# Kernel optimization log

Measured on AMD Instinct MI355X. Metric: run time of the kernel, lower is better.

## Reference

```python
import jax, jax.numpy as jnp
import numpy as np

VOCAB = 50257   # N_max = len(word_to_idx)
IN_DIM = 256
HID = 13        # forced: out Linear in_features = 2*hidden_dim must equal dec output 2*13
L = 2048


def _lstm_dir(seq, Wih, Whh, b, reverse):
    """Single-direction LSTM over seq [T, F] with zero init. b = b_ih + b_hh.
    Torch gate order: i, f, g, o."""
    H = Whh.shape[1]

    def step(carry, x_t):
        h, c = carry
        z = Wih @ x_t + Whh @ h + b                  # (4H,)
        i, f, g, o = jnp.split(z, 4)
        c2 = jax.nn.sigmoid(f) * c + jax.nn.sigmoid(i) * jnp.tanh(g)
        h2 = jax.nn.sigmoid(o) * jnp.tanh(c2)
        return (h2, c2), h2

    init = (jnp.zeros((H,), seq.dtype), jnp.zeros((H,), seq.dtype))
    (hn, cn), hs = jax.lax.scan(step, init, seq, reverse=reverse)
    return hs, hn, cn


def _dec_cell(x_scalar, h, c, Wih, Whh, b):
    """One LSTM cell step with scalar input (input_size=1). Returns new h."""
    z = Wih[:, 0] * x_scalar + Whh @ h + b
    i, f, g, o = jnp.split(z, 4)
    c2 = jax.nn.sigmoid(f) * c + jax.nn.sigmoid(i) * jnp.tanh(g)
    return jax.nn.sigmoid(o) * jnp.tanh(c2)


def setup_inputs() -> dict:
    key = jax.random.key(0)
    ks = jax.random.split(key, 16)
    s = 0.05
    G = 4 * HID  # 52; also num_layers*2*HID = 52 (proj in_features)
    return {
        "x": jax.random.randint(ks[0], (L,), 0, VOCAB),
        "emb_W": jax.random.normal(ks[1], (VOCAB + 1, IN_DIM)) * s,
        "enc_Wih0": jax.random.normal(ks[2], (2, G, IN_DIM)) * s,   # [dir, 4H, in]
        "enc_Whh0": jax.random.normal(ks[3], (2, G, HID)) * s,
        "enc_b0": jax.random.normal(ks[4], (2, G)) * s,
        "enc_Wih1": jax.random.normal(ks[5], (2, G, 2 * HID)) * s,  # layer1 input = 2*HID
        "enc_Whh1": jax.random.normal(ks[6], (2, G, HID)) * s,
        "enc_b1": jax.random.normal(ks[7], (2, G)) * s,
        "proj1_W": jax.random.normal(ks[8], (2 * HID, 2 * 2 * HID)) * s,
        "proj1_b": jax.random.normal(ks[9], (2 * HID,)) * s,
        "proj2_W": jax.random.normal(ks[10], (2 * HID, 2 * 2 * HID)) * s,
        "proj2_b": jax.random.normal(ks[11], (2 * HID,)) * s,
        "dec_Wih": jax.random.normal(ks[12], (2, G, 1)) * s,
        "dec_Whh": jax.random.normal(ks[13], (2, G, HID)) * s,
        "dec_b": jax.random.normal(ks[14], (2, G)) * s,
        "out_W": jax.random.normal(ks[15], (VOCAB, 2 * HID)) * s,
        "out_b": jnp.zeros((VOCAB,), jnp.float32),
    }


def reference(x, emb_W, enc_Wih0, enc_Whh0, enc_b0, enc_Wih1, enc_Whh1, enc_b1,
              proj1_W, proj1_b, proj2_W, proj2_b, dec_Wih, dec_Whh, dec_b,
              out_W, out_b):
    embs = emb_W[x]                                            # (L, IN_DIM)

    # Encoder: 2-layer bidirectional LSTM, batch=1 (vectors).
    hs_f0, hnf0, cnf0 = _lstm_dir(embs, enc_Wih0[0], enc_Whh0[0], enc_b0[0], False)
    hs_b0, hnb0, cnb0 = _lstm_dir(embs, enc_Wih0[1], enc_Whh0[1], enc_b0[1], True)
    out0 = jnp.concatenate([hs_f0, hs_b0], axis=-1)            # (L, 2*HID)
    _, hnf1, cnf1 = _lstm_dir(out0, enc_Wih1[0], enc_Whh1[0], enc_b1[0], False)
    _, hnb1, cnb1 = _lstm_dir(out0, enc_Wih1[1], enc_Whh1[1], enc_b1[1], True)

    # torch h_n layout: [l0_fwd, l0_bwd, l1_fwd, l1_bwd]
    h_flat = jnp.concatenate([hnf0, hnb0, hnf1, hnb1])         # (52,)
    c_flat = jnp.concatenate([cnf0, cnb0, cnf1, cnb1])
    state_h = (proj1_W @ h_flat + proj1_b).reshape(2, HID)     # dec (dir, HID) init
    state_c = (proj2_W @ c_flat + proj2_b).reshape(2, HID)

    # Decoder step 0: input -1.0 with projected initial state.
    start = jnp.float32(-1.0)
    step0 = jnp.concatenate([
        _dec_cell(start, state_h[0], state_c[0], dec_Wih[0], dec_Whh[0], dec_b[0]),
        _dec_cell(start, state_h[1], state_c[1], dec_Wih[1], dec_Whh[1], dec_b[1]),
    ])                                                          # (26,)

    # Steps i>0: original code calls self.dec(input) with NO hidden state, so each
    # step uses zero initial state and depends only on x[i-1] -> fully parallel.
    xs = x[:-1].astype(jnp.float32)                             # (L-1,)
    z0 = jnp.zeros((HID,), jnp.float32)
    rest = jax.vmap(lambda v: jnp.concatenate([
        _dec_cell(v, z0, z0, dec_Wih[0], dec_Whh[0], dec_b[0]),
        _dec_cell(v, z0, z0, dec_Wih[1], dec_Whh[1], dec_b[1]),
    ]))(xs)                                                     # (L-1, 26)

    dec_out = jnp.concatenate([step0[None, :], rest], axis=0)   # (L, 26)
    preds = dec_out @ out_W.T + out_b                           # (L, VOCAB)
    return preds, embs
```

## Files before the change

### kernel.cpp

```cpp
#include <hip/hip_runtime.h>
#include <hip/hip_bf16.h>
#include <cstdint>
#include <cstddef>

#define L      2048
#define IN_DIM 256
#define HID    13
#define G      52
#define VOCAB  50257
#define PRED_N ((size_t)L * VOCAB)
#define L2E    1.4426950408889634f
#define INV2L2E 0.34657359027997264f
#define NTX    50
#define NTILE  (NTX * 16)
#define GB     254

static __device__ __forceinline__ float fexp2(float x) { return __builtin_amdgcn_exp2f(x); }
static __device__ __forceinline__ float frcp(float x) { return __builtin_amdgcn_rcpf(x); }
static __device__ __forceinline__ float sigm(float z) { return 1.f - frcp(fexp2(z * L2E) + 1.f); }
static __device__ __forceinline__ float tanh_(float z) { return 1.f - 2.f * frcp(fexp2(z * (2.f * L2E)) + 1.f); }
static __device__ __forceinline__ float bcast(float v, int l) {
    return __int_as_float(__builtin_amdgcn_readlane(__float_as_int(v), l));
}

__global__ void __launch_bounds__(64) k_probe_dep(float* __restrict__ o)
{
    float a = 1.0f + threadIdx.x * 1e-6f;
    #pragma unroll 16
    for (int i = 0; i < 4096; ++i) a = fmaf(a, 1.0000001f, 1e-9f);
    o[threadIdx.x] = a;
}
__global__ void __launch_bounds__(64) k_probe_ilp(float* __restrict__ o)
{
    float a0 = 1.f, a1 = 1.1f, a2 = 1.2f, a3 = 1.3f, a4 = 1.4f, a5 = 1.5f, a6 = 1.6f, a7 = 1.7f;
    #pragma unroll 8
    for (int i = 0; i < 512; ++i) {
        a0 = fmaf(a0, 1.0000001f, 1e-9f); a1 = fmaf(a1, 1.0000001f, 1e-9f);
        a2 = fmaf(a2, 1.0000001f, 1e-9f); a3 = fmaf(a3, 1.0000001f, 1e-9f);
        a4 = fmaf(a4, 1.0000001f, 1e-9f); a5 = fmaf(a5, 1.0000001f, 1e-9f);
        a6 = fmaf(a6, 1.0000001f, 1e-9f); a7 = fmaf(a7, 1.0000001f, 1e-9f);
    }
    o[64 + threadIdx.x] = ((a0 + a1) + (a2 + a3)) + ((a4 + a5) + (a6 + a7));
}

__global__ void __launch_bounds__(160) k_emb_u0(
    const int* __restrict__ x, const float* __restrict__ embW,
    const float* __restrict__ Wih0, const float* __restrict__ b0,
    const float* __restrict__ dWih, const float* __restrict__ db,
    float* __restrict__ out_embs, float* __restrict__ u0, float* __restrict__ dec)
{
    __shared__ float se[IN_DIM];
    int t = blockIdx.x;
    int tid = threadIdx.x;
    if (tid < 128) {
        int rowx = x[t];
        float2 e = ((const float2*)(embW + (size_t)rowx * IN_DIM))[tid];
        se[2 * tid]     = e.x;
        se[2 * tid + 1] = e.y;
        ((float2*)(out_embs + (size_t)t * IN_DIM))[tid] = e;
    }
    __syncthreads();
    if (tid < 2 * G) {
        int dirg = tid / G, g = tid % G;
        int gate = g / HID, row = g % HID;
        float msc = (gate == 2) ? 2.f * L2E : L2E;
        float acc = b0[dirg * G + g];
        const float* w = Wih0 + (size_t)(dirg * G + g) * IN_DIM;
        #pragma unroll 8
        for (int k = 0; k < IN_DIM; ++k)
            acc = fmaf(w[k], se[k], acc);
        u0[((size_t)dirg * L + t) * 64 + gate * 16 + row] = msc * acc;
    } else if (tid < 128) {
        int p = tid - 2 * G;
        int dirp = p / 12, pp = p % 12;
        int gate = pp / 3, row = HID + pp % 3;
        u0[((size_t)dirp * L + t) * 64 + gate * 16 + row] = 0.f;
    } else if (tid < 128 + 2 * HID && t >= 1) {
        int j = tid - 128;
        int dir = j / HID, jj = j % HID;
        float v = (float)x[t - 1];
        int base = dir * G;
        float zi = fmaf(dWih[base + jj],           v, db[base + jj]);
        float zg = fmaf(dWih[base + 2 * HID + jj], v, db[base + 2 * HID + jj]);
        float zo = fmaf(dWih[base + 3 * HID + jj], v, db[base + 3 * HID + jj]);
        float c2 = sigm(zi) * tanh_(zg);
        dec[(size_t)t * (2 * HID) + j] = sigm(zo) * tanh_(c2);
    }
}

static __device__ __forceinline__ void compute8(
    const float* buf, const float* whh, float kcv, float onev,
    bool m16, bool m32, float& h, float& c, float* h8)
{
    #pragma unroll
    for (int k = 0; k < 8; ++k) {
        float h0 = bcast(h, 0), h1 = bcast(h, 1), h2 = bcast(h, 2), h3 = bcast(h, 3);
        float h4 = bcast(h, 4), h5 = bcast(h, 5), h6 = bcast(h, 6), h7 = bcast(h, 7);
        float h8_ = bcast(h, 8), h9 = bcast(h, 9), h10 = bcast(h, 10), h11 = bcast(h, 11);
        float h12 = bcast(h, 12);
        float A = fmaf(whh[0], h0, buf[k]);
        float B = whh[1] * h1;
        A = fmaf(whh[2],  h2,  A);  B = fmaf(whh[3],  h3,  B);
        A = fmaf(whh[4],  h4,  A);  B = fmaf(whh[5],  h5,  B);
        A = fmaf(whh[6],  h6,  A);  B = fmaf(whh[7],  h7,  B);
        A = fmaf(whh[8],  h8_, A);  B = fmaf(whh[9],  h9,  B);
        A = fmaf(whh[10], h10, A);  B = fmaf(whh[11], h11, B);
        A = fmaf(whh[12], h12, A);
        float z = A + B;
        float act = fmaf(-kcv, frcp(fexp2(z) + 1.f), onev);
        float pa = act, pb = act;
        asm("s_nop 1\n\tv_permlane16_swap_b32 %0, %1" : "+v"(pa), "+v"(pb));
        float sf = m16 ? pa : pb;
        float qa = act, qb = act;
        asm("s_nop 1\n\tv_permlane32_swap_b32 %0, %1" : "+v"(qa), "+v"(qb));
        float tg = m32 ? qa : qb;
        float ra = tg, rb = tg;
        asm("s_nop 1\n\tv_permlane16_swap_b32 %0, %1" : "+v"(ra), "+v"(rb));
        float so = m16 ? ra : rb;
        float c2 = fmaf(sf, c, act * tg);
        float th = fmaf(-2.f, frcp(fexp2(c2) + 1.f), 1.f);
        h = so * th;
        c = c2;
        h8[k] = h;
    }
}

template<bool DOUT>
static __device__ __forceinline__ void chain_core(
    const float* ub, int pstep, const float* whh, float kcv, float onev,
    bool m16, bool m32, float* outp, float& hout, float& cout)
{
    float bufA[8], bufB[8], h8[8];
    float h = 0.f, c = 0.f;
    #pragma unroll
    for (int k = 0; k < 8; ++k) bufA[k] = ub[k * pstep];
    #pragma unroll
    for (int k = 0; k < 8; ++k) bufB[k] = ub[(8 + k) * pstep];

    for (int tcb = 0; tcb < L; tcb += 16) {
        compute8(bufA, whh, kcv, onev, m16, m32, h, c, h8);
        if (DOUT) {
            #pragma unroll
            for (int k = 0; k < 8; ++k) outp[k * pstep] = h8[k];
            outp += 8 * pstep;
        }
        if (tcb + 16 < L) {
            #pragma unroll
            for (int k = 0; k < 8; ++k) bufA[k] = ub[(tcb + 16 + k) * pstep];
        }
        compute8(bufB, whh, kcv, onev, m16, m32, h, c, h8);
        if (DOUT) {
            #pragma unroll
            for (int k = 0; k < 8; ++k) outp[k * pstep] = h8[k];
            outp += 8 * pstep;
        }
        if (tcb + 24 < L) {
            #pragma unroll
            for (int k = 0; k < 8; ++k) bufB[k] = ub[(tcb + 24 + k) * pstep];
        }
    }
    hout = h; cout = c;
}

template<bool DOUT>
static __device__ __forceinline__ void run_chain(
    const float* u, const float* Whh, float* out0p,
    float* finh, float* finc, int chain_base, int dir, int lane)
{
    int lg16 = lane & 15, gate = lane >> 4;
    int rsrc = gate * HID + (lg16 < HID ? lg16 : HID - 1);
    float kcv, onev;
    if (gate == 2)      { kcv = 2.f;        onev = 1.f; }
    else if (gate == 0) { kcv = 2.f * L2E;  onev = 2.f * L2E; }
    else                { kcv = 1.f;        onev = 1.f; }
    float msc = (gate == 2) ? 2.f * L2E : L2E;
    float whh[HID];
    #pragma unroll
    for (int k = 0; k < HID; ++k) whh[k] = msc * Whh[(dir * G + rsrc) * HID + k];

    int ia = lane, ib = lane;
    asm("s_nop 1\n\tv_permlane16_swap_b32 %0, %1" : "+v"(ia), "+v"(ib));
    bool m16 = (ia == (lane ^ 16));
    int ja = lane, jb = lane;
    asm("s_nop 1\n\tv_permlane32_swap_b32 %0, %1" : "+v"(ja), "+v"(jb));
    bool m32 = (ja == (lane ^ 32));

    const float* ub = u + (size_t)dir * L * 64 + (dir ? (size_t)(L - 1) * 64 : 0) + lane;
    int pstep = dir ? -64 : 64;
    float* outp = out0p ? out0p + ((size_t)dir * L + (dir ? L - 1 : 0)) * 64 + lane : (float*)nullptr;

    float h, c;
    chain_core<DOUT>(ub, pstep, whh, kcv, onev, m16, m32, outp, h, c);

    if (lane < HID) {
        finh[(chain_base + dir) * HID + lane] = h;
        finc[(chain_base + dir) * HID + lane] = c * INV2L2E;
    }
}

__global__ void __launch_bounds__(512) k_phase0(
    const float* __restrict__ u, const float* __restrict__ Whh,
    float* __restrict__ out0p, float* __restrict__ finh, float* __restrict__ finc,
    const float* __restrict__ dec, const float* __restrict__ outW,
    const float* __restrict__ outb, float* __restrict__ preds)
{
    __shared__ float sd[128][28];
    int bid = blockIdx.x;
    int tid = threadIdx.x;
    if (bid < 2) {
        if (tid >= 64) return;
        __builtin_amdgcn_s_setprio(3);
        run_chain<true>(u, Whh, out0p, finh, finc, 0, bid, tid);
        return;
    }
    __builtin_amdgcn_s_setprio(0);
    int b = bid - 2;
    const int q = NTILE / GB, r = NTILE % GB;
    int start = b * q + (b < r ? b : r);
    int cnt   = q + (b < r ? 1 : 0);
    for (int tt = 0; tt < cnt; ++tt) {
        int tile = start + tt;
        int ix = tile % NTX, iy = tile / NTX;
        int nbase = ix * 1024, i0 = iy * 128;
        __syncthreads();
        for (int li = tid; li < 128 * 26; li += 512) {
            int rr = li / 26, cc = li % 26;
            sd[rr][cc] = dec[(size_t)(i0 + rr) * 26 + cc];
        }
        __syncthreads();
        int n0 = nbase + tid, n1 = nbase + 512 + tid;
        bool a0 = n0 < VOCAB, a1 = n1 < VOCAB;
        float w0[26], w1[26], b0v = 0.f, b1v = 0.f;
        #pragma unroll
        for (int k = 0; k < 26; ++k) { w0[k] = 0.f; w1[k] = 0.f; }
        if (a0) { const float* w = outW + (size_t)n0 * 26;
            #pragma unroll
            for (int k = 0; k < 26; ++k) w0[k] = w[k];
            b0v = outb[n0]; }
        if (a1) { const float* w = outW + (size_t)n1 * 26;
            #pragma unroll
            for (int k = 0; k < 26; ++k) w1[k] = w[k];
            b1v = outb[n1]; }
        for (int i = 0; i < 128; ++i) {
            int grow = i0 + i;
            float acc0 = b0v, acc1 = b1v;
            const float* dr = sd[i];
            #pragma unroll
            for (int k = 0; k < 26; ++k) {
                float d = dr[k];
                acc0 = fmaf(d, w0[k], acc0);
                acc1 = fmaf(d, w1[k], acc1);
            }
            if (grow != 0) {
                size_t rb = (size_t)grow * VOCAB;
                if (a0) preds[rb + n0] = acc0;
                if (a1) preds[rb + n1] = acc1;
            }
        }
    }
}

__global__ void k_u1(const float* __restrict__ out0p, const float* __restrict__ Wih1,
                     const float* __restrict__ b1, float* __restrict__ u1)
{
    int idx = blockIdx.x * blockDim.x + threadIdx.x;
    if (idx >= L * 2 * 64) return;
    int t    = idx >> 7;
    int remv = idx & 127;
    int d1   = remv >> 6;
    int lane = remv & 63;
    int gate = lane >> 4, row = lane & 15;
    size_t oidx = ((size_t)d1 * L + t) * 64 + lane;
    if (row >= HID) { u1[oidx] = 0.f; return; }
    int g = gate * HID + row;
    float msc = (gate == 2) ? 2.f * L2E : L2E;
    float acc = b1[d1 * G + g];
    const float* w = Wih1 + (size_t)(d1 * G + g) * (2 * HID);
    const float* o0 = out0p + (size_t)t * 64;
    const float* o1 = out0p + ((size_t)L + t) * 64;
    #pragma unroll
    for (int k = 0; k < HID; ++k)
        acc = fmaf(w[k], o0[k], acc);
    #pragma unroll
    for (int k = 0; k < HID; ++k)
        acc = fmaf(w[HID + k], o1[k], acc);
    u1[oidx] = msc * acc;
}

__global__ void __launch_bounds__(64) k_phase1(
    const float* __restrict__ u, const float* __restrict__ Whh,
    float* __restrict__ finh, float* __restrict__ finc)
{
    run_chain<false>(u, Whh, (float*)nullptr, finh, finc, 2, blockIdx.x, threadIdx.x);
}

__global__ void __launch_bounds__(64) k_final(const float* __restrict__ fin_h, const float* __restrict__ fin_c,
                                              const float* __restrict__ p1W, const float* __restrict__ p1b,
                                              const float* __restrict__ p2W, const float* __restrict__ p2b,
                                              const float* __restrict__ dWih, const float* __restrict__ dWhh,
                                              const float* __restrict__ db, float* __restrict__ dec)
{
    __shared__ float sh[2 * HID], sc[2 * HID], sz[G];
    int tid = threadIdx.x;
    if (tid < 4 * HID) {
        int r = tid < 2 * HID ? tid : tid - 2 * HID;
        const float* W   = tid < 2 * HID ? p1W : p2W;
        const float* src = tid < 2 * HID ? fin_h : fin_c;
        float acc = tid < 2 * HID ? p1b[r] : p2b[r];
        for (int k = 0; k < 4 * HID; ++k) acc = fmaf(W[r * 4 * HID + k], src[k], acc);
        if (tid < 2 * HID) sh[r] = acc; else sc[r] = acc;
    }
    __syncthreads();
    for (int dir = 0; dir < 2; ++dir) {
        if (tid < G) {
            float acc = db[dir * G + tid] - dWih[dir * G + tid];
            for (int k = 0; k < HID; ++k)
                acc = fmaf(dWhh[(dir * G + tid) * HID + k], sh[dir * HID + k], acc);
            sz[tid] = acc;
        }
        __syncthreads();
        if (tid < HID) {
            float si = sigm(sz[tid]);
            float sf = sigm(sz[HID + tid]);
            float tg = tanh_(sz[2 * HID + tid]);
            float so = sigm(sz[3 * HID + tid]);
            float c2 = fmaf(sf, sc[dir * HID + tid], si * tg);
            dec[dir * HID + tid] = so * tanh_(c2);
        }
        __syncthreads();
    }
}

__global__ void k_row0(const float* __restrict__ dec, const float* __restrict__ outW,
                       const float* __restrict__ outb, float* __restrict__ preds)
{
    int n = blockIdx.x * blockDim.x + threadIdx.x;
    if (n >= VOCAB) return;
    float acc = outb[n];
    const float* w = outW + (size_t)n * 26;
    #pragma unroll
    for (int k = 0; k < 26; ++k) acc = fmaf(w[k], dec[k], acc);
    preds[n] = acc;
}

extern "C" void kernel_launch(void* const* d_in, const int* in_sizes, int n_in,
                              void* d_out, int out_size, void* d_ws, size_t ws_size,
                              hipStream_t stream)
{
    (void)in_sizes; (void)n_in; (void)out_size; (void)ws_size;

    const int*   x     = (const int*)d_in[0];
    const float* embW  = (const float*)d_in[1];
    const float* eWih0 = (const float*)d_in[2];
    const float* eWhh0 = (const float*)d_in[3];
    const float* eb0   = (const float*)d_in[4];
    const float* eWih1 = (const float*)d_in[5];
    const float* eWhh1 = (const float*)d_in[6];
    const float* eb1   = (const float*)d_in[7];
    const float* p1W   = (const float*)d_in[8];
    const float* p1b   = (const float*)d_in[9];
    const float* p2W   = (const float*)d_in[10];
    const float* p2b   = (const float*)d_in[11];
    const float* dWih  = (const float*)d_in[12];
    const float* dWhh  = (const float*)d_in[13];
    const float* db    = (const float*)d_in[14];
    const float* outW  = (const float*)d_in[15];
    const float* outb  = (const float*)d_in[16];

    float* ws    = (float*)d_ws;
    float* u0    = ws;
    float* u1    = u0 + 2 * L * 64;
    float* out0p = u1 + 2 * L * 64;
    float* dec   = out0p + 2 * L * 64;
    float* fin_h = dec + L * 2 * HID;
    float* fin_c = fin_h + 64;
    float* probe = fin_c + 64;

    float* preds    = (float*)d_out;
    float* out_embs = preds + PRED_N;

    hipLaunchKernelGGL(k_probe_dep, dim3(1), dim3(64), 0, stream, probe);
    hipLaunchKernelGGL(k_probe_ilp, dim3(1), dim3(64), 0, stream, probe);

    hipLaunchKernelGGL(k_emb_u0, dim3(L), dim3(160), 0, stream,
                       x, embW, eWih0, eb0, dWih, db, out_embs, u0, dec);

    hipLaunchKernelGGL(k_phase0, dim3(2 + GB), dim3(512), 0, stream,
                       u0, eWhh0, out0p, fin_h, fin_c,
                       dec, outW, outb, preds);

    hipLaunchKernelGGL(k_u1, dim3((L * 2 * 64 + 255) / 256), dim3(256), 0, stream,
                       out0p, eWih1, eb1, u1);

    hipLaunchKernelGGL(k_phase1, dim3(2), dim3(64), 0, stream,
                       u1, eWhh1, fin_h, fin_c);

    hipLaunchKernelGGL(k_final, dim3(1), dim3(64), 0, stream,
                       fin_h, fin_c, p1W, p1b, p2W, p2b, dWih, dWhh, db, dec);

    hipLaunchKernelGGL(k_row0, dim3((VOCAB + 255) / 256), dim3(256), 0, stream,
                       dec, outW, outb, preds);
}
```

Measured before the change: 617.2 us.

## Remove probe kernels, widen phase0 blocks, split recurrence FMA chain

```diff
diff --git a/kernel.cpp b/kernel.cpp
--- a/kernel.cpp
+++ b/kernel.cpp
@@ -11,9 +11,10 @@
 #define PRED_N ((size_t)L * VOCAB)
 #define L2E    1.4426950408889634f
 #define INV2L2E 0.34657359027997264f
-#define NTX    50
+#define NTX    25
 #define NTILE  (NTX * 16)
 #define GB     254
+#define DYNLDS 49152
 
 static __device__ __forceinline__ float fexp2(float x) { return __builtin_amdgcn_exp2f(x); }
 static __device__ __forceinline__ float frcp(float x) { return __builtin_amdgcn_rcpf(x); }
@@ -21,26 +22,6 @@
 static __device__ __forceinline__ float tanh_(float z) { return 1.f - 2.f * frcp(fexp2(z * (2.f * L2E)) + 1.f); }
 static __device__ __forceinline__ float bcast(float v, int l) {
     return __int_as_float(__builtin_amdgcn_readlane(__float_as_int(v), l));
-}
-
-__global__ void __launch_bounds__(64) k_probe_dep(float* __restrict__ o)
-{
-    float a = 1.0f + threadIdx.x * 1e-6f;
-    #pragma unroll 16
-    for (int i = 0; i < 4096; ++i) a = fmaf(a, 1.0000001f, 1e-9f);
-    o[threadIdx.x] = a;
-}
-__global__ void __launch_bounds__(64) k_probe_ilp(float* __restrict__ o)
-{
-    float a0 = 1.f, a1 = 1.1f, a2 = 1.2f, a3 = 1.3f, a4 = 1.4f, a5 = 1.5f, a6 = 1.6f, a7 = 1.7f;
-    #pragma unroll 8
-    for (int i = 0; i < 512; ++i) {
-        a0 = fmaf(a0, 1.0000001f, 1e-9f); a1 = fmaf(a1, 1.0000001f, 1e-9f);
-        a2 = fmaf(a2, 1.0000001f, 1e-9f); a3 = fmaf(a3, 1.0000001f, 1e-9f);
-        a4 = fmaf(a4, 1.0000001f, 1e-9f); a5 = fmaf(a5, 1.0000001f, 1e-9f);
-        a6 = fmaf(a6, 1.0000001f, 1e-9f); a7 = fmaf(a7, 1.0000001f, 1e-9f);
-    }
-    o[64 + threadIdx.x] = ((a0 + a1) + (a2 + a3)) + ((a4 + a5) + (a6 + a7));
 }
 
 __global__ void __launch_bounds__(160) k_emb_u0(
@@ -88,9 +69,10 @@
     }
 }
 
+template<bool DOUT>
 static __device__ __forceinline__ void compute8(
     const float* buf, const float* whh, float kcv, float onev,
-    bool m16, bool m32, float& h, float& c, float* h8)
+    bool m16, bool m32, float& h, float& c, float* outp, int pstep)
 {
     #pragma unroll
     for (int k = 0; k < 8; ++k) {
@@ -100,13 +82,14 @@
         float h12 = bcast(h, 12);
         float A = fmaf(whh[0], h0, buf[k]);
         float B = whh[1] * h1;
-        A = fmaf(whh[2],  h2,  A);  B = fmaf(whh[3],  h3,  B);
-        A = fmaf(whh[4],  h4,  A);  B = fmaf(whh[5],  h5,  B);
-        A = fmaf(whh[6],  h6,  A);  B = fmaf(whh[7],  h7,  B);
-        A = fmaf(whh[8],  h8_, A);  B = fmaf(whh[9],  h9,  B);
-        A = fmaf(whh[10], h10, A);  B = fmaf(whh[11], h11, B);
+        float C = whh[2] * h2;
+        float D = whh[3] * h3;
+        A = fmaf(whh[4], h4, A);   B = fmaf(whh[5], h5, B);
+        C = fmaf(whh[6], h6, C);   D = fmaf(whh[7], h7, D);
+        A = fmaf(whh[8], h8_, A);  B = fmaf(whh[9], h9, B);
+        C = fmaf(whh[10], h10, C); D = fmaf(whh[11], h11, D);
         A = fmaf(whh[12], h12, A);
-        float z = A + B;
+        float z = (A + B) + (C + D);
         float act = fmaf(-kcv, frcp(fexp2(z) + 1.f), onev);
         float pa = act, pb = act;
         asm("s_nop 1\n\tv_permlane16_swap_b32 %0, %1" : "+v"(pa), "+v"(pb));
@@ -121,7 +104,7 @@
         float th = fmaf(-2.f, frcp(fexp2(c2) + 1.f), 1.f);
         h = so * th;
         c = c2;
-        h8[k] = h;
+        if (DOUT) outp[k * pstep] = h;
     }
 }
 
@@ -130,7 +113,7 @@
     const float* ub, int pstep, const float* whh, float kcv, float onev,
     bool m16, bool m32, float* outp, float& hout, float& cout)
 {
-    float bufA[8], bufB[8], h8[8];
+    float bufA[8], bufB[8];
     float h = 0.f, c = 0.f;
     #pragma unroll
     for (int k = 0; k < 8; ++k) bufA[k] = ub[k * pstep];
@@ -138,22 +121,14 @@
     for (int k = 0; k < 8; ++k) bufB[k] = ub[(8 + k) * pstep];
 
     for (int tcb = 0; tcb < L; tcb += 16) {
-        compute8(bufA, whh, kcv, onev, m16, m32, h, c, h8);
-        if (DOUT) {
-            #pragma unroll
-            for (int k = 0; k < 8; ++k) outp[k * pstep] = h8[k];
-            outp += 8 * pstep;
-        }
+        compute8<DOUT>(bufA, whh, kcv, onev, m16, m32, h, c, outp, pstep);
+        if (DOUT) outp += 8 * pstep;
         if (tcb + 16 < L) {
             #pragma unroll
             for (int k = 0; k < 8; ++k) bufA[k] = ub[(tcb + 16 + k) * pstep];
         }
-        compute8(bufB, whh, kcv, onev, m16, m32, h, c, h8);
-        if (DOUT) {
-            #pragma unroll
-            for (int k = 0; k < 8; ++k) outp[k * pstep] = h8[k];
-            outp += 8 * pstep;
-        }
+        compute8<DOUT>(bufB, whh, kcv, onev, m16, m32, h, c, outp, pstep);
+        if (DOUT) outp += 8 * pstep;
         if (tcb + 24 < L) {
             #pragma unroll
             for (int k = 0; k < 8; ++k) bufB[k] = ub[(tcb + 24 + k) * pstep];
@@ -198,13 +173,13 @@
     }
 }
 
-__global__ void __launch_bounds__(512) k_phase0(
+__global__ void __launch_bounds__(1024) k_phase0(
     const float* __restrict__ u, const float* __restrict__ Whh,
     float* __restrict__ out0p, float* __restrict__ finh, float* __restrict__ finc,
     const float* __restrict__ dec, const float* __restrict__ outW,
     const float* __restrict__ outb, float* __restrict__ preds)
 {
-    __shared__ float sd[128][28];
+    extern __shared__ float sd[];
     int bid = blockIdx.x;
     int tid = threadIdx.x;
     if (bid < 2) {
@@ -221,14 +196,14 @@
     for (int tt = 0; tt < cnt; ++tt) {
         int tile = start + tt;
         int ix = tile % NTX, iy = tile / NTX;
-        int nbase = ix * 1024, i0 = iy * 128;
+        int nbase = ix * 2048, i0 = iy * 128;
         __syncthreads();
-        for (int li = tid; li < 128 * 26; li += 512) {
+        for (int li = tid; li < 128 * 26; li += 1024) {
             int rr = li / 26, cc = li % 26;
-            sd[rr][cc] = dec[(size_t)(i0 + rr) * 26 + cc];
+            sd[rr * 28 + cc] = dec[(size_t)(i0 + rr) * 26 + cc];
         }
         __syncthreads();
-        int n0 = nbase + tid, n1 = nbase + 512 + tid;
+        int n0 = nbase + tid, n1 = nbase + 1024 + tid;
         bool a0 = n0 < VOCAB, a1 = n1 < VOCAB;
         float w0[26], w1[26], b0v = 0.f, b1v = 0.f;
         #pragma unroll
@@ -244,7 +219,7 @@
         for (int i = 0; i < 128; ++i) {
             int grow = i0 + i;
             float acc0 = b0v, acc1 = b1v;
-            const float* dr = sd[i];
+            const float* dr = sd + i * 28;
             #pragma unroll
             for (int k = 0; k < 26; ++k) {
                 float d = dr[k];
@@ -374,18 +349,14 @@
     float* dec   = out0p + 2 * L * 64;
     float* fin_h = dec + L * 2 * HID;
     float* fin_c = fin_h + 64;
-    float* probe = fin_c + 64;
 
     float* preds    = (float*)d_out;
     float* out_embs = preds + PRED_N;
 
-    hipLaunchKernelGGL(k_probe_dep, dim3(1), dim3(64), 0, stream, probe);
-    hipLaunchKernelGGL(k_probe_ilp, dim3(1), dim3(64), 0, stream, probe);
-
     hipLaunchKernelGGL(k_emb_u0, dim3(L), dim3(160), 0, stream,
                        x, embW, eWih0, eb0, dWih, db, out_embs, u0, dec);
 
-    hipLaunchKernelGGL(k_phase0, dim3(2 + GB), dim3(512), 0, stream,
+    hipLaunchKernelGGL(k_phase0, dim3(2 + GB), dim3(1024), DYNLDS, stream,
                        u0, eWhh0, out0p, fin_h, fin_c,
                        dec, outW, outb, preds);
 
```

After: 616.2 us. No clear change (-0.2%).
